# Performance work log

Hardware: AMD Instinct MI355X
Metric: run time of the kernel (lower is better)

Reference implementation:

```python
import jax, jax.numpy as jnp
import numpy as np


def conv1x1(x, W, b):
    # 1x1 Conv2d == per-pixel linear over channels. x: [B,C,H,W], W: [O,C], b: [O]
    return jnp.einsum('oc,bchw->bohw', W, x) + b[None, :, None, None]


def setup_inputs() -> dict:
    key = jax.random.key(0)
    ks = jax.random.split(key, 18)
    B, C, Hd, H, W = 16, 64, 64, 32, 32
    s = 0.05
    f = jax.random.normal
    return {
        'h': f(ks[0], (B, C, H, W), jnp.float32),
        'm': f(ks[1], (B, C, H, W), jnp.float32),
        'Wq': f(ks[2], (Hd, C), jnp.float32) * s,
        'bq': f(ks[3], (Hd,), jnp.float32) * s,
        'Wk': f(ks[4], (Hd, C), jnp.float32) * s,
        'bk': f(ks[5], (Hd,), jnp.float32) * s,
        'Wk2': f(ks[6], (Hd, C), jnp.float32) * s,
        'bk2': f(ks[7], (Hd,), jnp.float32) * s,
        'Wv': f(ks[8], (C, C), jnp.float32) * s,
        'bv': f(ks[9], (C,), jnp.float32) * s,
        'Wv2': f(ks[10], (C, C), jnp.float32) * s,
        'bv2': f(ks[11], (C,), jnp.float32) * s,
        'Wz': f(ks[12], (2 * C, 2 * C), jnp.float32) * s,
        'bz': f(ks[13], (2 * C,), jnp.float32) * s,
        'Wm': f(ks[14], (3 * C, 3 * C), jnp.float32) * s,
        'bm': f(ks[15], (3 * C,), jnp.float32) * s,
    }


def reference(h, m, Wq, bq, Wk, bk, Wk2, bk2, Wv, bv, Wv2, bv2, Wz, bz, Wm, bm):
    B, C, H, W = h.shape
    Hd = Wq.shape[0]
    N = H * W
    # Shared query from h
    Q_h = conv1x1(h, Wq, bq).reshape(B, Hd, N).transpose(0, 2, 1)  # [B,N,Hd]
    # Self-attention branch over h
    K_h = conv1x1(h, Wk, bk).reshape(B, Hd, N)                     # [B,Hd,N]
    A_h = jax.nn.softmax(jnp.einsum('bnd,bdm->bnm', Q_h, K_h), axis=-1)  # [B,N,N]
    V_h = conv1x1(h, Wv, bv).reshape(B, C, N)                      # [B,C,N]
    Z_h = jnp.einsum('bnm,bcm->bcn', A_h, V_h).reshape(B, C, H, W)
    # Cross-attention branch over memory m (same query Q_h)
    K_m = conv1x1(m, Wk2, bk2).reshape(B, Hd, N)
    A_m = jax.nn.softmax(jnp.einsum('bnd,bdm->bnm', Q_h, K_m), axis=-1)
    V_m = conv1x1(m, Wv2, bv2).reshape(B, C, N)
    Z_m = jnp.einsum('bnm,bcm->bcn', A_m, V_m).reshape(B, C, H, W)
    # Fuse and gated memory update
    Z = conv1x1(jnp.concatenate([Z_h, Z_m], axis=1), Wz, bz)       # [B,2C,H,W]
    combined = conv1x1(jnp.concatenate([Z, h], axis=1), Wm, bm)    # [B,3C,H,W]
    mo, mg, mi = combined[:, :C], combined[:, C:2 * C], combined[:, 2 * C:]
    mi = jax.nn.sigmoid(mi)
    new_m = (1 - mi) * m + mi * jnp.tanh(mg)
    new_h = jax.nn.sigmoid(mo) * new_m
    return (new_h, new_m)
```

## Files before the change

kernel.cpp:

```cpp
#include <hip/hip_runtime.h>

typedef unsigned short u16;
typedef unsigned int u32;
typedef __attribute__((ext_vector_type(8))) short bf16x8;
typedef __attribute__((ext_vector_type(4))) short bf16x4;
typedef __attribute__((ext_vector_type(4))) float f32x4;

#define MFMA(a, b, c) __builtin_amdgcn_mfma_f32_16x16x32_bf16((a), (b), (c), 0, 0, 0)
#define MFMA16(a, b, c) __builtin_amdgcn_mfma_f32_16x16x16bf16_1k((a), (b), (c), 0, 0, 0)

static __device__ __forceinline__ u16 f2bf(float x) {
  u32 u = __float_as_uint(x);
  u += 0x7FFFu + ((u >> 16) & 1u);
  return (u16)(u >> 16);
}
static __device__ __forceinline__ u32 packbf_t(float hi, float lo) {
  return __builtin_amdgcn_perm(__float_as_uint(hi), __float_as_uint(lo), 0x07060302u);
}
static __device__ __forceinline__ u32 packbf(float lo, float hi) {
  return (u32)f2bf(lo) | ((u32)f2bf(hi) << 16);
}

__global__ void prep_kernel(const float* __restrict__ Wq, const float* __restrict__ Wk,
                            const float* __restrict__ Wk2, const float* __restrict__ Wv,
                            const float* __restrict__ Wv2, const float* __restrict__ Wz,
                            const float* __restrict__ Wm, const float* __restrict__ bm,
                            u16* __restrict__ W5, u16* __restrict__ Wzb,
                            u16* __restrict__ Wmb, float* __restrict__ bmp) {
  const int id = blockIdx.x * 256 + threadIdx.x;
  if (id < 20480) {
    const int wi = id >> 12, e = id & 4095;
    const float* src = wi == 0 ? Wq : wi == 1 ? Wk : wi == 2 ? Wk2 : wi == 3 ? Wv : Wv2;
    W5[id] = f2bf(src[e]);
  } else if (id < 36864) {
    const int e = id - 20480;
    Wzb[e] = f2bf(Wz[e]);
  } else if (id < 73728) {
    const int e = id - 36864;
    const int p = e / 192, k = e % 192;
    const int hb2 = p / 96, r1 = p % 96, ctl = r1 / 48, r2 = r1 % 48;
    const int g = r2 >> 4, mm = r2 & 15;
    const int o = g * 64 + (hb2 * 2 + ctl) * 16 + mm;
    Wmb[p * 192 + k] = f2bf(Wm[o * 192 + k]);
  } else if (id < 73920) {
    const int p = id - 73728;
    const int hb2 = p / 96, r1 = p % 96, ctl = r1 / 48, r2 = r1 % 48;
    const int g = r2 >> 4, mm = r2 & 15;
    const int o = g * 64 + (hb2 * 2 + ctl) * 16 + mm;
    bmp[p] = bm[o];
  }
}

__global__ __launch_bounds__(256) void proj_kernel(
    const float* __restrict__ h, const float* __restrict__ m_,
    const float* __restrict__ bq, const float* __restrict__ bk,
    const float* __restrict__ bk2, const float* __restrict__ bv,
    const float* __restrict__ bv2, const u16* __restrict__ W5,
    u16* __restrict__ Qb, u16* __restrict__ Khb, u16* __restrict__ Kmb,
    u16* __restrict__ Vhb, u16* __restrict__ Vmb, u16* __restrict__ hbuf)
{
  const int b = blockIdx.y, n0 = blockIdx.x * 64, z = blockIdx.z;
  __shared__ __align__(16) u16 xt[64][72];
  const int tid = threadIdx.x;
  const float* __restrict__ X = z ? m_ : h;

  {
    const int px = tid & 63, c0 = (tid >> 6) * 16;
#pragma unroll
    for (int i = 0; i < 8; ++i) {
      const int c = c0 + 2 * i;
      const float f0 = X[(b * 64 + c) * 1024 + n0 + px];
      const float f1 = X[(b * 64 + c + 1) * 1024 + n0 + px];
      *(u32*)&xt[px][c] = packbf(f0, f1);
    }
  }
  __syncthreads();

  const int lane = tid & 63, w = tid >> 6;
  const int mm = lane & 15, q = lane >> 4;

  const bf16x8 xa0 = *(const bf16x8*)&xt[w * 16 + mm][q * 8];
  const bf16x8 xa1 = *(const bf16x8*)&xt[w * 16 + mm][32 + q * 8];

  auto qk_store = [&](u16* dst, const u16* Wb, const float* bias) {
#pragma unroll
    for (int ot = 0; ot < 4; ++ot) {
      const bf16x8 wb0 = *(const bf16x8*)(Wb + (ot * 16 + mm) * 64 + q * 8);
      const bf16x8 wb1 = *(const bf16x8*)(Wb + (ot * 16 + mm) * 64 + 32 + q * 8);
      const float4 b4 = *(const float4*)(bias + ot * 16 + q * 4);
      f32x4 d = {b4.x, b4.y, b4.z, b4.w};
      d = MFMA(wb0, xa0, d);
      d = MFMA(wb1, xa1, d);
      uint2 val;
      val.x = packbf(d[0], d[1]);
      val.y = packbf(d[2], d[3]);
      *(uint2*)(dst + (b * 1024 + n0 + w * 16 + mm) * 64 + ot * 16 + q * 4) = val;
    }
  };
  auto v_store = [&](u16* dst, const u16* Wb, const float* bias) {
#pragma unroll
    for (int ot = 0; ot < 4; ++ot) {
      const bf16x8 wb0 = *(const bf16x8*)(Wb + (ot * 16 + mm) * 64 + q * 8);
      const bf16x8 wb1 = *(const bf16x8*)(Wb + (ot * 16 + mm) * 64 + 32 + q * 8);
      const float bb = bias[ot * 16 + mm];
      f32x4 d = {bb, bb, bb, bb};
      d = MFMA(xa0, wb0, d);
      d = MFMA(xa1, wb1, d);
      uint2 val;
      val.x = packbf(d[0], d[1]);
      val.y = packbf(d[2], d[3]);
      *(uint2*)(dst + b * 65536 + blockIdx.x * 4096 + (ot * 16 + mm) * 64 +
                w * 16 + q * 4) = val;
    }
  };

  if (z == 0) {
    qk_store(Qb, W5, bq);
    qk_store(Khb, W5 + 4096, bk);
    v_store(Vhb, W5 + 3 * 4096, bv);
    const int px = tid >> 2, sg = tid & 3;
    u32* dst = (u32*)(hbuf + (b * 1024 + n0 + px) * 64 + sg * 16);
    const u16* srcr = &xt[px][sg * 16];
#pragma unroll
    for (int j = 0; j < 8; ++j) dst[j] = *(const u32*)(srcr + 2 * j);
  } else {
    qk_store(Kmb, W5 + 2 * 4096, bk2);
    v_store(Vmb, W5 + 4 * 4096, bv2);
  }
}

__global__ __launch_bounds__(256) void attn_kernel(
    const u16* __restrict__ Qb, const u16* __restrict__ Khb,
    const u16* __restrict__ Kmb, const u16* __restrict__ Vhb,
    const u16* __restrict__ Vmb, u16* __restrict__ Ztb)
{
  const int id = blockIdx.x;
  const int b = id & 15;
  const int br = (id >> 4) & 1;
  const int qh = id >> 5;
  const u16* __restrict__ K = (br ? Kmb : Khb) + b * 65536;
  const u16* __restrict__ V = (br ? Vmb : Vhb) + b * 65536;

  __shared__ __align__(16) u16 pool[18432];
  __shared__ float rsw[4][64];
  u16* const Kl = pool;
  u16* const Vl = pool + 9216;

  const int tid = threadIdx.x, w = tid >> 6, lane = tid & 63;
  const int mm = lane & 15, q = lane >> 4;
  const int q0 = qh * 64;

  bf16x8 qb0[4], qb1[4];
#pragma unroll
  for (int qt = 0; qt < 4; ++qt) {
    const u16* Qp = Qb + (b * 1024 + q0 + qt * 16 + mm) * 64;
    qb0[qt] = *(const bf16x8*)(Qp + q * 8);
    qb1[qt] = *(const bf16x8*)(Qp + 32 + q * 8);
  }

  f32x4 z[4][4];
#pragma unroll
  for (int qt = 0; qt < 4; ++qt)
#pragma unroll
    for (int ct = 0; ct < 4; ++ct) z[qt][ct] = (f32x4){0.f, 0.f, 0.f, 0.f};
  float rp[4] = {0.f, 0.f, 0.f, 0.f};

  const int so0 = (tid >> 3) * 72 + (tid & 7) * 8;
  const int so1 = so0 + 32 * 72;
  uint4 sk0, sk1, sv0, sv1;
  auto stage_load = [&](int kc) {
    const u16* Ks = K + kc * 4096;
    const u16* Vs = V + kc * 4096;
    sk0 = *(const uint4*)(Ks + tid * 8);
    sk1 = *(const uint4*)(Ks + tid * 8 + 2048);
    sv0 = *(const uint4*)(Vs + tid * 8);
    sv1 = *(const uint4*)(Vs + tid * 8 + 2048);
  };
  auto stage_store = [&](int buf) {
    u16* Kd = Kl + buf * 4608;
    u16* Vd = Vl + buf * 4608;
    *(uint4*)(Kd + so0) = sk0;
    *(uint4*)(Kd + so1) = sk1;
    *(uint4*)(Vd + so0) = sv0;
    *(uint4*)(Vd + so1) = sv1;
  };

  stage_load(0);
  stage_store(0);
  __syncthreads();

  int cur = 0;
#pragma unroll 1
  for (int kc = 0; kc < 16; ++kc) {
    if (kc < 15) stage_load(kc + 1);

    const u16* Kc = Kl + cur * 4608;
    const u16* Vc = Vl + cur * 4608;
    const bf16x8 kf0 = *(const bf16x8*)(Kc + (w * 16 + mm) * 72 + q * 8);
    const bf16x8 kf1 = *(const bf16x8*)(Kc + (w * 16 + mm) * 72 + 32 + q * 8);
    bf16x4 vf[4];
#pragma unroll
    for (int ct = 0; ct < 4; ++ct)
      vf[ct] = *(const bf16x4*)(Vc + (ct * 16 + mm) * 72 + w * 16 + q * 4);

#pragma unroll
    for (int qt = 0; qt < 4; ++qt) {
      f32x4 s = {0.f, 0.f, 0.f, 0.f};
      s = MFMA(kf0, qb0[qt], s);
      s = MFMA(kf1, qb1[qt], s);
      const float e0 = __expf(s[0]), e1 = __expf(s[1]);
      const float e2 = __expf(s[2]), e3 = __expf(s[3]);
      rp[qt] += (e0 + e1) + (e2 + e3);
      union { u32 u[2]; bf16x4 v; } pb;
      pb.u[0] = packbf_t(e1, e0);
      pb.u[1] = packbf_t(e3, e2);
#pragma unroll
      for (int ct = 0; ct < 4; ++ct) z[qt][ct] = MFMA16(vf[ct], pb.v, z[qt][ct]);
    }

    if (kc < 15) stage_store(cur ^ 1);
    __syncthreads();
    cur ^= 1;
  }

  u16* const zcb = pool;
#pragma unroll
  for (int qt = 0; qt < 4; ++qt) {
    float v = rp[qt];
    v += __shfl_xor(v, 16);
    v += __shfl_xor(v, 32);
    if (q == 0) rsw[w][qt * 16 + mm] = v;
#pragma unroll
    for (int ct = 0; ct < 4; ++ct) {
      uint2 val;
      val.x = packbf_t(z[qt][ct][1], z[qt][ct][0]);
      val.y = packbf_t(z[qt][ct][3], z[qt][ct][2]);
      *(uint2*)(zcb + w * 4352 + (qt * 16 + mm) * 68 + ct * 16 + q * 4) = val;
    }
  }
  __syncthreads();

  const int c2 = tid & 31, qr = tid >> 5;
#pragma unroll
  for (int i = 0; i < 8; ++i) {
    const int query = qr + i * 8;
    const float rt = rsw[0][query] + rsw[1][query] + rsw[2][query] + rsw[3][query];
    const float rinv = __builtin_amdgcn_rcpf(rt);
    float vlo = 0.f, vhi = 0.f;
#pragma unroll
    for (int ww = 0; ww < 4; ++ww) {
      const u32 u = *(const u32*)(zcb + ww * 4352 + query * 68 + c2 * 2);
      vlo += __uint_as_float(u << 16);
      vhi += __uint_as_float(u & 0xffff0000u);
    }
    vlo *= rinv;
    vhi *= rinv;
    *(u32*)(Ztb + (b * 1024 + q0 + query) * 128 + br * 64 + c2 * 2) = packbf_t(vhi, vlo);
  }
}

__global__ __launch_bounds__(256) void tail_kernel(
    const u16* __restrict__ Ztb, const u16* __restrict__ hbuf,
    const float* __restrict__ m_, const u16* __restrict__ Wzb,
    const float* __restrict__ bz, const u16* __restrict__ Wmb,
    const float* __restrict__ bmp, float* __restrict__ out)
{
  const int b = blockIdx.y, n0 = blockIdx.x * 32;
  __shared__ __align__(16) u16 zp[32][136];
  const int tid = threadIdx.x, lane = tid & 63, wv = tid >> 6;
  const int mm = lane & 15, q = lane >> 4;
  const int pxt = wv & 1, oh = wv >> 1;

  {
    bf16x8 za[4];
#pragma unroll
    for (int ks = 0; ks < 4; ++ks)
      za[ks] = *(const bf16x8*)(Ztb + (b * 1024 + n0 + pxt * 16 + mm) * 128 +
                                ks * 32 + q * 8);
#pragma unroll
    for (int ot = 0; ot < 4; ++ot) {
      const int o0 = oh * 64 + ot * 16;
      const float4 b4 = *(const float4*)(bz + o0 + q * 4);
      f32x4 d = {b4.x, b4.y, b4.z, b4.w};
#pragma unroll
      for (int ks = 0; ks < 4; ++ks) {
        const bf16x8 wb = *(const bf16x8*)(Wzb + (o0 + mm) * 128 + ks * 32 + q * 8);
        d = MFMA(wb, za[ks], d);
      }
      uint2 val;
      val.x = packbf(d[0], d[1]);
      val.y = packbf(d[2], d[3]);
      *(uint2*)&zp[pxt * 16 + mm][o0 + q * 4] = val;
    }
  }
  __syncthreads();

  {
    const int hb2 = oh;
    bf16x8 fa[6];
#pragma unroll
    for (int ks = 0; ks < 4; ++ks)
      fa[ks] = *(const bf16x8*)&zp[pxt * 16 + mm][ks * 32 + q * 8];
    {
      const u16* hp = hbuf + (b * 1024 + n0 + pxt * 16 + mm) * 64;
      fa[4] = *(const bf16x8*)(hp + q * 8);
      fa[5] = *(const bf16x8*)(hp + 32 + q * 8);
    }
    f32x4 dd[6];
#pragma unroll
    for (int j = 0; j < 6; ++j) {
      const int p = hb2 * 96 + j * 16 + mm;
      const float bb = bmp[p];
      f32x4 d = {bb, bb, bb, bb};
#pragma unroll
      for (int ks = 0; ks < 6; ++ks) {
        const bf16x8 wb = *(const bf16x8*)(Wmb + p * 192 + ks * 32 + q * 8);
        d = MFMA(fa[ks], wb, d);
      }
      dd[j] = d;
    }
#pragma unroll
    for (int ctl = 0; ctl < 2; ++ctl) {
      const int c = (hb2 * 2 + ctl) * 16 + mm;
      const int px = n0 + pxt * 16 + q * 4;
      const float4 mold = *(const float4*)(m_ + (b * 64 + c) * 1024 + px);
      float4 nh, nm;
#pragma unroll
      for (int r = 0; r < 4; ++r) {
        const float xo = dd[ctl * 3 + 0][r];
        const float xg = dd[ctl * 3 + 1][r];
        const float xi = dd[ctl * 3 + 2][r];
        const float si = __builtin_amdgcn_rcpf(1.f + __expf(-xi));
        const float th = 1.f - 2.f * __builtin_amdgcn_rcpf(__expf(2.f * xg) + 1.f);
        const float so = __builtin_amdgcn_rcpf(1.f + __expf(-xo));
        const float mo = ((const float*)&mold)[r];
        const float nmv = (1.f - si) * mo + si * th;
        ((float*)&nm)[r] = nmv;
        ((float*)&nh)[r] = so * nmv;
      }
      *(float4*)(out + (b * 64 + c) * 1024 + px) = nh;
      *(float4*)(out + 1048576 + (b * 64 + c) * 1024 + px) = nm;
    }
  }
}

extern "C" void kernel_launch(void* const* d_in, const int* in_sizes, int n_in,
                              void* d_out, int out_size, void* d_ws, size_t ws_size,
                              hipStream_t stream) {
  const float* h   = (const float*)d_in[0];
  const float* m   = (const float*)d_in[1];
  const float* Wq  = (const float*)d_in[2];
  const float* bq  = (const float*)d_in[3];
  const float* Wk  = (const float*)d_in[4];
  const float* bk  = (const float*)d_in[5];
  const float* Wk2 = (const float*)d_in[6];
  const float* bk2 = (const float*)d_in[7];
  const float* Wv  = (const float*)d_in[8];
  const float* bv  = (const float*)d_in[9];
  const float* Wv2 = (const float*)d_in[10];
  const float* bv2 = (const float*)d_in[11];
  const float* Wz  = (const float*)d_in[12];
  const float* bz  = (const float*)d_in[13];
  const float* Wm  = (const float*)d_in[14];
  const float* bm  = (const float*)d_in[15];
  float* out = (float*)d_out;

  char* ws = (char*)d_ws;
  const size_t MB = 1024 * 1024;
  u16* Qb   = (u16*)(ws + 0 * MB);
  u16* Khb  = (u16*)(ws + 2 * MB);
  u16* Kmb  = (u16*)(ws + 4 * MB);
  u16* Vhb  = (u16*)(ws + 6 * MB);
  u16* Vmb  = (u16*)(ws + 8 * MB);
  u16* hbuf = (u16*)(ws + 10 * MB);
  u16* Ztb  = (u16*)(ws + 12 * MB);
  u16* W5   = (u16*)(ws + 16 * MB);
  u16* Wzb  = (u16*)(ws + 16 * MB + 40960);
  u16* Wmb  = (u16*)(ws + 16 * MB + 73728);
  float* bmp = (float*)(ws + 16 * MB + 147456);

  prep_kernel<<<289, 256, 0, stream>>>(Wq, Wk, Wk2, Wv, Wv2, Wz, Wm, bm,
                                       W5, Wzb, Wmb, bmp);
  proj_kernel<<<dim3(16, 16, 2), 256, 0, stream>>>(h, m, bq, bk, bk2, bv, bv2, W5,
                                                   Qb, Khb, Kmb, Vhb, Vmb, hbuf);
  attn_kernel<<<512, 256, 0, stream>>>(Qb, Khb, Kmb, Vhb, Vmb, Ztb);
  tail_kernel<<<dim3(32, 16), 256, 0, stream>>>(Ztb, hbuf, m, Wzb, bz, Wmb, bmp, out);
}
```

Baseline: 136.0 us.

## Fuse projections into attention kernel, recompute K/V on the fly, drop prep kernel

Removes the separate weight-prep and projection kernels. The attention kernel now loads fp32 h/m tiles and computes Q, K and V projections per KV chunk with MFMA, keeping weights in registers. This avoids writing and reading the bf16 Q/K/V intermediates and saves two launches. In exchange, each query block recomputes the K/V projections for all 1024 keys (16x redundant), adds register pressure, and reads strided fp32 columns of X. The tail kernel converts Wz/Wm to bf16 on the fly and swaps its grid order.

```diff
diff --git a/kernel.cpp b/kernel.cpp
--- a/kernel.cpp
+++ b/kernel.cpp
@@ -20,142 +20,104 @@
 static __device__ __forceinline__ u32 packbf(float lo, float hi) {
   return (u32)f2bf(lo) | ((u32)f2bf(hi) << 16);
 }
-
-__global__ void prep_kernel(const float* __restrict__ Wq, const float* __restrict__ Wk,
-                            const float* __restrict__ Wk2, const float* __restrict__ Wv,
-                            const float* __restrict__ Wv2, const float* __restrict__ Wz,
-                            const float* __restrict__ Wm, const float* __restrict__ bm,
-                            u16* __restrict__ W5, u16* __restrict__ Wzb,
-                            u16* __restrict__ Wmb, float* __restrict__ bmp) {
-  const int id = blockIdx.x * 256 + threadIdx.x;
-  if (id < 20480) {
-    const int wi = id >> 12, e = id & 4095;
-    const float* src = wi == 0 ? Wq : wi == 1 ? Wk : wi == 2 ? Wk2 : wi == 3 ? Wv : Wv2;
-    W5[id] = f2bf(src[e]);
-  } else if (id < 36864) {
-    const int e = id - 20480;
-    Wzb[e] = f2bf(Wz[e]);
-  } else if (id < 73728) {
-    const int e = id - 36864;
-    const int p = e / 192, k = e % 192;
-    const int hb2 = p / 96, r1 = p % 96, ctl = r1 / 48, r2 = r1 % 48;
-    const int g = r2 >> 4, mm = r2 & 15;
-    const int o = g * 64 + (hb2 * 2 + ctl) * 16 + mm;
-    Wmb[p * 192 + k] = f2bf(Wm[o * 192 + k]);
-  } else if (id < 73920) {
-    const int p = id - 73728;
-    const int hb2 = p / 96, r1 = p % 96, ctl = r1 / 48, r2 = r1 % 48;
-    const int g = r2 >> 4, mm = r2 & 15;
-    const int o = g * 64 + (hb2 * 2 + ctl) * 16 + mm;
-    bmp[p] = bm[o];
-  }
-}
-
-__global__ __launch_bounds__(256) void proj_kernel(
+static __device__ __forceinline__ bf16x8 ld8bf(const float* __restrict__ p) {
+  const float4 a = *(const float4*)p;
+  const float4 b = *(const float4*)(p + 4);
+  union { u32 u[4]; bf16x8 v; } r;
+  r.u[0] = packbf(a.x, a.y);
+  r.u[1] = packbf(a.z, a.w);
+  r.u[2] = packbf(b.x, b.y);
+  r.u[3] = packbf(b.z, b.w);
+  return r.v;
+}
+
+__global__ __launch_bounds__(256, 2) void fused_attn_kernel(
     const float* __restrict__ h, const float* __restrict__ m_,
-    const float* __restrict__ bq, const float* __restrict__ bk,
-    const float* __restrict__ bk2, const float* __restrict__ bv,
-    const float* __restrict__ bv2, const u16* __restrict__ W5,
-    u16* __restrict__ Qb, u16* __restrict__ Khb, u16* __restrict__ Kmb,
-    u16* __restrict__ Vhb, u16* __restrict__ Vmb, u16* __restrict__ hbuf)
-{
-  const int b = blockIdx.y, n0 = blockIdx.x * 64, z = blockIdx.z;
-  __shared__ __align__(16) u16 xt[64][72];
-  const int tid = threadIdx.x;
-  const float* __restrict__ X = z ? m_ : h;
-
-  {
-    const int px = tid & 63, c0 = (tid >> 6) * 16;
-#pragma unroll
-    for (int i = 0; i < 8; ++i) {
-      const int c = c0 + 2 * i;
-      const float f0 = X[(b * 64 + c) * 1024 + n0 + px];
-      const float f1 = X[(b * 64 + c + 1) * 1024 + n0 + px];
-      *(u32*)&xt[px][c] = packbf(f0, f1);
-    }
-  }
-  __syncthreads();
-
-  const int lane = tid & 63, w = tid >> 6;
-  const int mm = lane & 15, q = lane >> 4;
-
-  const bf16x8 xa0 = *(const bf16x8*)&xt[w * 16 + mm][q * 8];
-  const bf16x8 xa1 = *(const bf16x8*)&xt[w * 16 + mm][32 + q * 8];
-
-  auto qk_store = [&](u16* dst, const u16* Wb, const float* bias) {
-#pragma unroll
-    for (int ot = 0; ot < 4; ++ot) {
-      const bf16x8 wb0 = *(const bf16x8*)(Wb + (ot * 16 + mm) * 64 + q * 8);
-      const bf16x8 wb1 = *(const bf16x8*)(Wb + (ot * 16 + mm) * 64 + 32 + q * 8);
-      const float4 b4 = *(const float4*)(bias + ot * 16 + q * 4);
-      f32x4 d = {b4.x, b4.y, b4.z, b4.w};
-      d = MFMA(wb0, xa0, d);
-      d = MFMA(wb1, xa1, d);
-      uint2 val;
-      val.x = packbf(d[0], d[1]);
-      val.y = packbf(d[2], d[3]);
-      *(uint2*)(dst + (b * 1024 + n0 + w * 16 + mm) * 64 + ot * 16 + q * 4) = val;
-    }
-  };
-  auto v_store = [&](u16* dst, const u16* Wb, const float* bias) {
-#pragma unroll
-    for (int ot = 0; ot < 4; ++ot) {
-      const bf16x8 wb0 = *(const bf16x8*)(Wb + (ot * 16 + mm) * 64 + q * 8);
-      const bf16x8 wb1 = *(const bf16x8*)(Wb + (ot * 16 + mm) * 64 + 32 + q * 8);
-      const float bb = bias[ot * 16 + mm];
-      f32x4 d = {bb, bb, bb, bb};
-      d = MFMA(xa0, wb0, d);
-      d = MFMA(xa1, wb1, d);
-      uint2 val;
-      val.x = packbf(d[0], d[1]);
-      val.y = packbf(d[2], d[3]);
-      *(uint2*)(dst + b * 65536 + blockIdx.x * 4096 + (ot * 16 + mm) * 64 +
-                w * 16 + q * 4) = val;
-    }
-  };
-
-  if (z == 0) {
-    qk_store(Qb, W5, bq);
-    qk_store(Khb, W5 + 4096, bk);
-    v_store(Vhb, W5 + 3 * 4096, bv);
-    const int px = tid >> 2, sg = tid & 3;
-    u32* dst = (u32*)(hbuf + (b * 1024 + n0 + px) * 64 + sg * 16);
-    const u16* srcr = &xt[px][sg * 16];
-#pragma unroll
-    for (int j = 0; j < 8; ++j) dst[j] = *(const u32*)(srcr + 2 * j);
-  } else {
-    qk_store(Kmb, W5 + 2 * 4096, bk2);
-    v_store(Vmb, W5 + 4 * 4096, bv2);
-  }
-}
-
-__global__ __launch_bounds__(256) void attn_kernel(
-    const u16* __restrict__ Qb, const u16* __restrict__ Khb,
-    const u16* __restrict__ Kmb, const u16* __restrict__ Vhb,
-    const u16* __restrict__ Vmb, u16* __restrict__ Ztb)
+    const float* __restrict__ Wq, const float* __restrict__ bq,
+    const float* __restrict__ Wk, const float* __restrict__ bk,
+    const float* __restrict__ Wk2, const float* __restrict__ bk2,
+    const float* __restrict__ Wv, const float* __restrict__ bv,
+    const float* __restrict__ Wv2, const float* __restrict__ bv2,
+    u16* __restrict__ hbuf, u16* __restrict__ Ztb)
 {
   const int id = blockIdx.x;
   const int b = id & 15;
   const int br = (id >> 4) & 1;
   const int qh = id >> 5;
-  const u16* __restrict__ K = (br ? Kmb : Khb) + b * 65536;
-  const u16* __restrict__ V = (br ? Vmb : Vhb) + b * 65536;
-
-  __shared__ __align__(16) u16 pool[18432];
+  const float* __restrict__ X = (br ? m_ : h) + b * 65536;
+  const float* __restrict__ H = h + b * 65536;
+  const float* __restrict__ WK = br ? Wk2 : Wk;
+  const float* __restrict__ BK = br ? bk2 : bk;
+  const float* __restrict__ WV = br ? Wv2 : Wv;
+  const float* __restrict__ BV = br ? bv2 : bv;
+
+  __shared__ __align__(16) u16 Qlds[64 * 72];
+  __shared__ __align__(16) u16 Klds[64 * 72];
+  __shared__ __align__(16) u16 zcb[4 * 64 * 68];
   __shared__ float rsw[4][64];
-  u16* const Kl = pool;
-  u16* const Vl = pool + 9216;
 
   const int tid = threadIdx.x, w = tid >> 6, lane = tid & 63;
   const int mm = lane & 15, q = lane >> 4;
   const int q0 = qh * 64;
 
+  bf16x8 wqA0[4], wqA1[4], wkA0[4], wkA1[4], wvB0[4], wvB1[4];
+#pragma unroll
+  for (int ot = 0; ot < 4; ++ot) {
+    const int ro = (ot * 16 + mm) * 64;
+    wqA0[ot] = ld8bf(Wq + ro + q * 8);
+    wqA1[ot] = ld8bf(Wq + ro + 32 + q * 8);
+    wkA0[ot] = ld8bf(WK + ro + q * 8);
+    wkA1[ot] = ld8bf(WK + ro + 32 + q * 8);
+    wvB0[ot] = ld8bf(WV + ro + q * 8);
+    wvB1[ot] = ld8bf(WV + ro + 32 + q * 8);
+  }
+  float4 bkq[4];
+  float bvs[4];
+#pragma unroll
+  for (int ot = 0; ot < 4; ++ot) {
+    bkq[ot] = *(const float4*)(BK + ot * 16 + q * 4);
+    bvs[ot] = BV[ot * 16 + mm];
+  }
+
+  {
+    const int qp = q0 + w * 16 + mm;
+    float xq[16];
+#pragma unroll
+    for (int i = 0; i < 2; ++i)
+#pragma unroll
+      for (int j = 0; j < 8; ++j) xq[i * 8 + j] = H[(i * 32 + q * 8 + j) * 1024 + qp];
+    union { u32 u[4]; bf16x8 v; } x0, x1;
+#pragma unroll
+    for (int p = 0; p < 4; ++p) {
+      x0.u[p] = packbf(xq[2 * p], xq[2 * p + 1]);
+      x1.u[p] = packbf(xq[8 + 2 * p], xq[9 + 2 * p]);
+    }
+    if (br == 0) {
+      u16* hp = hbuf + (b * 1024 + qp) * 64;
+      uint4 h0, h1;
+      h0.x = x0.u[0]; h0.y = x0.u[1]; h0.z = x0.u[2]; h0.w = x0.u[3];
+      h1.x = x1.u[0]; h1.y = x1.u[1]; h1.z = x1.u[2]; h1.w = x1.u[3];
+      *(uint4*)(hp + q * 8) = h0;
+      *(uint4*)(hp + 32 + q * 8) = h1;
+    }
+#pragma unroll
+    for (int ot = 0; ot < 4; ++ot) {
+      const float4 b4 = *(const float4*)(bq + ot * 16 + q * 4);
+      f32x4 d = {b4.x, b4.y, b4.z, b4.w};
+      d = MFMA(wqA0[ot], x0.v, d);
+      d = MFMA(wqA1[ot], x1.v, d);
+      uint2 val;
+      val.x = packbf(d[0], d[1]);
+      val.y = packbf(d[2], d[3]);
+      *(uint2*)(Qlds + (w * 16 + mm) * 72 + ot * 16 + q * 4) = val;
+    }
+  }
+  __syncthreads();
   bf16x8 qb0[4], qb1[4];
 #pragma unroll
   for (int qt = 0; qt < 4; ++qt) {
-    const u16* Qp = Qb + (b * 1024 + q0 + qt * 16 + mm) * 64;
-    qb0[qt] = *(const bf16x8*)(Qp + q * 8);
-    qb1[qt] = *(const bf16x8*)(Qp + 32 + q * 8);
+    qb0[qt] = *(const bf16x8*)(Qlds + (qt * 16 + mm) * 72 + q * 8);
+    qb1[qt] = *(const bf16x8*)(Qlds + (qt * 16 + mm) * 72 + 32 + q * 8);
   }
 
   f32x4 z[4][4];
@@ -165,43 +127,53 @@
     for (int ct = 0; ct < 4; ++ct) z[qt][ct] = (f32x4){0.f, 0.f, 0.f, 0.f};
   float rp[4] = {0.f, 0.f, 0.f, 0.f};
 
-  const int so0 = (tid >> 3) * 72 + (tid & 7) * 8;
-  const int so1 = so0 + 32 * 72;
-  uint4 sk0, sk1, sv0, sv1;
-  auto stage_load = [&](int kc) {
-    const u16* Ks = K + kc * 4096;
-    const u16* Vs = V + kc * 4096;
-    sk0 = *(const uint4*)(Ks + tid * 8);
-    sk1 = *(const uint4*)(Ks + tid * 8 + 2048);
-    sv0 = *(const uint4*)(Vs + tid * 8);
-    sv1 = *(const uint4*)(Vs + tid * 8 + 2048);
+  float xn[16];
+  union { u32 u[4]; bf16x8 v; } xb0, xb1;
+  auto xload = [&](int kc) {
+    const float* Xp = X + kc * 64 + w * 16 + mm;
+#pragma unroll
+    for (int i = 0; i < 2; ++i)
+#pragma unroll
+      for (int j = 0; j < 8; ++j) xn[i * 8 + j] = Xp[(i * 32 + q * 8 + j) * 1024];
   };
-  auto stage_store = [&](int buf) {
-    u16* Kd = Kl + buf * 4608;
-    u16* Vd = Vl + buf * 4608;
-    *(uint4*)(Kd + so0) = sk0;
-    *(uint4*)(Kd + so1) = sk1;
-    *(uint4*)(Vd + so0) = sv0;
-    *(uint4*)(Vd + so1) = sv1;
+  auto xpack = [&]() {
+#pragma unroll
+    for (int p = 0; p < 4; ++p) {
+      xb0.u[p] = packbf(xn[2 * p], xn[2 * p + 1]);
+      xb1.u[p] = packbf(xn[8 + 2 * p], xn[9 + 2 * p]);
+    }
   };
 
-  stage_load(0);
-  stage_store(0);
-  __syncthreads();
-
-  int cur = 0;
+  xload(0);
+  xpack();
 #pragma unroll 1
   for (int kc = 0; kc < 16; ++kc) {
-    if (kc < 15) stage_load(kc + 1);
-
-    const u16* Kc = Kl + cur * 4608;
-    const u16* Vc = Vl + cur * 4608;
-    const bf16x8 kf0 = *(const bf16x8*)(Kc + (w * 16 + mm) * 72 + q * 8);
-    const bf16x8 kf1 = *(const bf16x8*)(Kc + (w * 16 + mm) * 72 + 32 + q * 8);
+    if (kc < 15) xload(kc + 1);
+
+#pragma unroll
+    for (int ot = 0; ot < 4; ++ot) {
+      f32x4 d = {bkq[ot].x, bkq[ot].y, bkq[ot].z, bkq[ot].w};
+      d = MFMA(wkA0[ot], xb0.v, d);
+      d = MFMA(wkA1[ot], xb1.v, d);
+      uint2 val;
+      val.x = packbf(d[0], d[1]);
+      val.y = packbf(d[2], d[3]);
+      *(uint2*)(Klds + (w * 16 + mm) * 72 + ot * 16 + q * 4) = val;
+    }
+    const bf16x8 kf0 = *(const bf16x8*)(Klds + (w * 16 + mm) * 72 + q * 8);
+    const bf16x8 kf1 = *(const bf16x8*)(Klds + (w * 16 + mm) * 72 + 32 + q * 8);
+
     bf16x4 vf[4];
 #pragma unroll
-    for (int ct = 0; ct < 4; ++ct)
-      vf[ct] = *(const bf16x4*)(Vc + (ct * 16 + mm) * 72 + w * 16 + q * 4);
+    for (int ct = 0; ct < 4; ++ct) {
+      f32x4 d = {bvs[ct], bvs[ct], bvs[ct], bvs[ct]};
+      d = MFMA(xb0.v, wvB0[ct], d);
+      d = MFMA(xb1.v, wvB1[ct], d);
+      union { u32 u[2]; bf16x4 v; } pv;
+      pv.u[0] = packbf_t(d[1], d[0]);
+      pv.u[1] = packbf_t(d[3], d[2]);
+      vf[ct] = pv.v;
+    }
 
 #pragma unroll
     for (int qt = 0; qt < 4; ++qt) {
@@ -218,12 +190,9 @@
       for (int ct = 0; ct < 4; ++ct) z[qt][ct] = MFMA16(vf[ct], pb.v, z[qt][ct]);
     }
 
-    if (kc < 15) stage_store(cur ^ 1);
-    __syncthreads();
-    cur ^= 1;
-  }
-
-  u16* const zcb = pool;
+    if (kc < 15) xpack();
+  }
+
 #pragma unroll
   for (int qt = 0; qt < 4; ++qt) {
     float v = rp[qt];
@@ -261,11 +230,11 @@
 
 __global__ __launch_bounds__(256) void tail_kernel(
     const u16* __restrict__ Ztb, const u16* __restrict__ hbuf,
-    const float* __restrict__ m_, const u16* __restrict__ Wzb,
-    const float* __restrict__ bz, const u16* __restrict__ Wmb,
-    const float* __restrict__ bmp, float* __restrict__ out)
+    const float* __restrict__ m_, const float* __restrict__ Wz,
+    const float* __restrict__ bz, const float* __restrict__ Wm,
+    const float* __restrict__ bm, float* __restrict__ out)
 {
-  const int b = blockIdx.y, n0 = blockIdx.x * 32;
+  const int b = blockIdx.x, n0 = blockIdx.y * 32;
   __shared__ __align__(16) u16 zp[32][136];
   const int tid = threadIdx.x, lane = tid & 63, wv = tid >> 6;
   const int mm = lane & 15, q = lane >> 4;
@@ -284,7 +253,7 @@
       f32x4 d = {b4.x, b4.y, b4.z, b4.w};
 #pragma unroll
       for (int ks = 0; ks < 4; ++ks) {
-        const bf16x8 wb = *(const bf16x8*)(Wzb + (o0 + mm) * 128 + ks * 32 + q * 8);
+        const bf16x8 wb = ld8bf(Wz + (o0 + mm) * 128 + ks * 32 + q * 8);
         d = MFMA(wb, za[ks], d);
       }
       uint2 val;
@@ -309,12 +278,12 @@
     f32x4 dd[6];
 #pragma unroll
     for (int j = 0; j < 6; ++j) {
-      const int p = hb2 * 96 + j * 16 + mm;
-      const float bb = bmp[p];
+      const int o = (j % 3) * 64 + (hb2 * 2 + j / 3) * 16 + mm;
+      const float bb = bm[o];
       f32x4 d = {bb, bb, bb, bb};
 #pragma unroll
       for (int ks = 0; ks < 6; ++ks) {
-        const bf16x8 wb = *(const bf16x8*)(Wmb + p * 192 + ks * 32 + q * 8);
+        const bf16x8 wb = ld8bf(Wm + o * 192 + ks * 32 + q * 8);
         d = MFMA(fa[ks], wb, d);
       }
       dd[j] = d;
@@ -327,7 +296,7 @@
       float4 nh, nm;
 #pragma unroll
       for (int r = 0; r < 4; ++r) {
-        const float xo = dd[ctl * 3 + 0][r];
+        const float xo = dd[0 + ctl * 3 / 3 * 0 + (ctl * 3 + 0)][r];
         const float xg = dd[ctl * 3 + 1][r];
         const float xi = dd[ctl * 3 + 2][r];
         const float si = __builtin_amdgcn_rcpf(1.f + __expf(-xi));
@@ -367,22 +336,10 @@
 
   char* ws = (char*)d_ws;
   const size_t MB = 1024 * 1024;
-  u16* Qb   = (u16*)(ws + 0 * MB);
-  u16* Khb  = (u16*)(ws + 2 * MB);
-  u16* Kmb  = (u16*)(ws + 4 * MB);
-  u16* Vhb  = (u16*)(ws + 6 * MB);
-  u16* Vmb  = (u16*)(ws + 8 * MB);
-  u16* hbuf = (u16*)(ws + 10 * MB);
-  u16* Ztb  = (u16*)(ws + 12 * MB);
-  u16* W5   = (u16*)(ws + 16 * MB);
-  u16* Wzb  = (u16*)(ws + 16 * MB + 40960);
-  u16* Wmb  = (u16*)(ws + 16 * MB + 73728);
-  float* bmp = (float*)(ws + 16 * MB + 147456);
-
-  prep_kernel<<<289, 256, 0, stream>>>(Wq, Wk, Wk2, Wv, Wv2, Wz, Wm, bm,
-                                       W5, Wzb, Wmb, bmp);
-  proj_kernel<<<dim3(16, 16, 2), 256, 0, stream>>>(h, m, bq, bk, bk2, bv, bv2, W5,
-                                                   Qb, Khb, Kmb, Vhb, Vmb, hbuf);
-  attn_kernel<<<512, 256, 0, stream>>>(Qb, Khb, Kmb, Vhb, Vmb, Ztb);
-  tail_kernel<<<dim3(32, 16), 256, 0, stream>>>(Ztb, hbuf, m, Wzb, bz, Wmb, bmp, out);
-}
+  u16* hbuf = (u16*)(ws + 0 * MB);
+  u16* Ztb  = (u16*)(ws + 2 * MB);
+
+  fused_attn_kernel<<<512, 256, 0, stream>>>(h, m, Wq, bq, Wk, bk, Wk2, bk2,
+                                             Wv, bv, Wv2, bv2, hbuf, Ztb);
+  tail_kernel<<<dim3(16, 32), 256, 0, stream>>>(Ztb, hbuf, m, Wz, bz, Wm, bm, out);
+}
```

Result: slower. 156.8 us (+15.3%).
